# Kernel optimization log

Measured on AMD Instinct MI355X. Metric: run time of the kernel, lower is better.

The kernel has to match this reference:

```python
import jax, jax.numpy as jnp
import numpy as np

M_INST = 64   # num_instances (labels 1..64; 0 = background)
L_ANCH = 8    # anchors per instance
C_DIM = 256   # anchor_dim == embed dim (num_mapping_layers=0, num_heads=1)
B, H, W = 8, 64, 64


def setup_inputs() -> dict:
    key = jax.random.key(0)
    ks = jax.random.split(key, 7)
    s = 1.0 / np.sqrt(C_DIM)
    return {
        "anchors": jax.random.normal(ks[0], (M_INST, L_ANCH, C_DIM), jnp.float32),
        "features": jax.random.normal(ks[1], (B, H, W, C_DIM), jnp.float32),
        "instances_in_view": jax.random.randint(ks[2], (B, H, W), 0, M_INST + 1, jnp.int32),
        # nn.MultiheadAttention packed in-projection and out-projection params
        "in_proj_w": jax.random.normal(ks[3], (3 * C_DIM, C_DIM), jnp.float32) * s,
        "in_proj_b": jax.random.normal(ks[4], (3 * C_DIM,), jnp.float32) * s,
        "out_w": jax.random.normal(ks[5], (C_DIM, C_DIM), jnp.float32) * s,
        "out_b": jax.random.normal(ks[6], (C_DIM,), jnp.float32) * s,
    }


def reference(anchors, features, instances_in_view, in_proj_w, in_proj_b, out_w, out_b):
    # Cross-attention anchor_type, Identity maps (num_mapping_layers=0, num_heads=1).
    # Each pixel (query) attends to the L anchors of its instance; padding in the
    # original pad_sequence pipeline never affects non-pad queries, so the
    # gather/pack -> MHA -> unmap -> residual-add pipeline reduces to per-pixel math.
    C = anchors.shape[-1]
    Wq, Wk, Wv = in_proj_w[:C], in_proj_w[C:2 * C], in_proj_w[2 * C:]
    bq, bk, bv = in_proj_b[:C], in_proj_b[C:2 * C], in_proj_b[2 * C:]

    # Project keys/values once per instance: (M, L, C)
    K = jnp.einsum('mlc,dc->mld', anchors, Wk) + bk
    V = jnp.einsum('mlc,dc->mld', anchors, Wv) + bv

    Bsz, Hh, Ww, _ = features.shape
    f = features.reshape(-1, C)                       # (N, C)
    lab = instances_in_view.reshape(-1)               # (N,) labels 0..M
    idx = jnp.maximum(lab - 1, 0)                     # anchor row per pixel

    q = f @ Wq.T + bq                                 # (N, C)
    Kg = K[idx]                                       # (N, L, C) irregular gather
    Vg = V[idx]                                       # (N, L, C)

    scale = 1.0 / np.sqrt(C).astype(np.float32)
    scores = jnp.einsum('nc,nlc->nl', q, Kg) * scale  # (N, L)
    attn = jax.nn.softmax(scores, axis=-1)
    o = jnp.einsum('nl,nlc->nc', attn, Vg)            # (N, C)
    o = o @ out_w.T + out_b                           # MHA out_proj

    # background (label 0) pixels get zero anchor feature; residual add
    o = jnp.where((lab > 0)[:, None], o, jnp.zeros((), o.dtype))
    out = f + o
    return out.reshape(Bsz, Hh, Ww, C)
```

## Files before the change

### kernel.cpp

```cpp
#include <hip/hip_runtime.h>
#include <stdint.h>

#define C_DIM   256
#define L_ANCH  8
#define M_INST  64
#define NPIX    32768
#define LDSTR   264
#define WSTR    40
#define TSTR    80

typedef __attribute__((ext_vector_type(8))) short  short8;
typedef __attribute__((ext_vector_type(4))) float  float4v;

__device__ __forceinline__ float bf2f(unsigned short b) {
    union { unsigned u; float f; } x; x.u = ((unsigned)b) << 16; return x.f;
}
__device__ __forceinline__ unsigned short f2bf(float f) {
    union { unsigned u; float f; } x; x.f = f;
    unsigned u = x.u;
    return (unsigned short)((u + 0x7FFFu + ((u >> 16) & 1u)) >> 16);
}
__device__ __forceinline__ ushort4 f4bf(float4 f) {
    ushort4 v; v.x = f2bf(f.x); v.y = f2bf(f.y); v.z = f2bf(f.z); v.w = f2bf(f.w);
    return v;
}

__global__ __launch_bounds__(256) void prep1_kernel(
    const float* __restrict__ anchors, const float* __restrict__ in_proj_w,
    const float* __restrict__ in_proj_b, const float* __restrict__ out_w,
    unsigned short* __restrict__ Kb, unsigned short* __restrict__ Vb,
    unsigned short* __restrict__ WqT, unsigned short* __restrict__ Owb)
{
    __shared__ unsigned short Abuf[32 * LDSTR];
    __shared__ unsigned short Wtile[4][64 * WSTR];
    __shared__ unsigned short Ttile[64 * TSTR];
    const int b = blockIdx.x, t = threadIdx.x;

    if (b >= 96) {
        const int tidx = b - 96;
        const int r0 = (tidx >> 2) * 64, c0 = (tidx & 3) * 64;
#pragma unroll
        for (int i = 0; i < 4; ++i) {
            int id = t + i * 256;
            int row = id >> 4, c4 = id & 15;
            float4 f = *(const float4*)&in_proj_w[(size_t)(r0 + row) * C_DIM + c0 + c4 * 4];
            Ttile[(c4 * 4 + 0) * TSTR + row] = f2bf(f.x);
            Ttile[(c4 * 4 + 1) * TSTR + row] = f2bf(f.y);
            Ttile[(c4 * 4 + 2) * TSTR + row] = f2bf(f.z);
            Ttile[(c4 * 4 + 3) * TSTR + row] = f2bf(f.w);
        }
        __syncthreads();
#pragma unroll
        for (int i = 0; i < 2; ++i) {
            int id = t + i * 256;
            int cc = id >> 3, ch = id & 7;
            *(short8*)&WqT[(size_t)(c0 + cc) * C_DIM + r0 + ch * 8] =
                *(const short8*)&Ttile[cc * TSTR + ch * 8];
        }
        return;
    }

    if (b >= 32) {
        const int id = (b - 32) * 256 + t;
        float4 f = *((const float4*)out_w + id);
        *((ushort4*)Owb + id) = f4bf(f);
        return;
    }

    const int mat = b >> 4, tile = b & 15, m0 = tile * 32;
#pragma unroll
    for (int i = 0; i < 8; ++i) {
        int id = t + i * 256;
        int row = id >> 6, c4 = id & 63;
        float4 f = *((const float4*)(anchors + (size_t)(m0 + row) * C_DIM) + c4);
        *(ushort4*)&Abuf[row * LDSTR + c4 * 4] = f4bf(f);
    }
    __syncthreads();

    const int wave = t >> 6, lane = t & 63, r16 = lane & 15, quad = lane >> 4;
    const int wbase = C_DIM + mat * C_DIM + wave * 64;
    unsigned short* Wl = &Wtile[wave][0];

    float4v acc[2][4];
#pragma unroll
    for (int mt = 0; mt < 2; ++mt)
#pragma unroll
        for (int nt = 0; nt < 4; ++nt)
#pragma unroll
            for (int r = 0; r < 4; ++r) acc[mt][nt][r] = 0.f;

    for (int ks = 0; ks < 8; ++ks) {
        const int rr = lane >> 3, cc = lane & 7;
#pragma unroll
        for (int i = 0; i < 8; ++i) {
            int row = rr + i * 8;
            float4 f = *((const float4*)(in_proj_w + (size_t)(wbase + row) * C_DIM + ks * 32) + cc);
            *(ushort4*)&Wl[row * WSTR + cc * 4] = f4bf(f);
        }
        const int c0 = ks * 32 + quad * 8;
        short8 afr[2], bfr[4];
#pragma unroll
        for (int mt = 0; mt < 2; ++mt)
            afr[mt] = *(const short8*)&Abuf[(mt * 16 + r16) * LDSTR + c0];
#pragma unroll
        for (int nt = 0; nt < 4; ++nt)
            bfr[nt] = *(const short8*)&Wl[(nt * 16 + r16) * WSTR + quad * 8];
#pragma unroll
        for (int mt = 0; mt < 2; ++mt)
#pragma unroll
            for (int nt = 0; nt < 4; ++nt)
                acc[mt][nt] = __builtin_amdgcn_mfma_f32_16x16x32_bf16(
                    afr[mt], bfr[nt], acc[mt][nt], 0, 0, 0);
    }

    unsigned short* dst = mat ? Vb : Kb;
#pragma unroll
    for (int nt = 0; nt < 4; ++nt) {
        const int col = wave * 64 + nt * 16 + r16;
        const float bias = in_proj_b[C_DIM + mat * C_DIM + col];
#pragma unroll
        for (int mt = 0; mt < 2; ++mt)
#pragma unroll
            for (int r = 0; r < 4; ++r) {
                int row = m0 + mt * 16 + quad * 4 + r;
                dst[(size_t)row * C_DIM + col] = f2bf(acc[mt][nt][r] + bias);
            }
    }
}

__global__ __launch_bounds__(256) void prep2_kernel(
    const unsigned short* __restrict__ Kb, const unsigned short* __restrict__ Vb,
    const unsigned short* __restrict__ WqT, const unsigned short* __restrict__ Owb,
    const float* __restrict__ in_proj_b,
    unsigned short* __restrict__ G, unsigned short* __restrict__ U,
    float* __restrict__ g0)
{
    __shared__ unsigned short Abuf[32 * LDSTR];
    const int b = blockIdx.x, t = threadIdx.x;
    const int isG = (b < 16) ? 1 : 0;
    const int tile = b & 15, m0 = tile * 32;
    const unsigned short* src = isG ? Kb : Vb;
    const unsigned short* W   = isG ? WqT : Owb;
    unsigned short* dst       = isG ? G : U;

#pragma unroll
    for (int i = 0; i < 4; ++i) {
        int id = t + i * 256;
        int row = id >> 5, c8 = id & 31;
        *(short8*)&Abuf[row * LDSTR + c8 * 8] =
            *(const short8*)&src[(size_t)(m0 + row) * C_DIM + c8 * 8];
    }
    __syncthreads();

    const int wave = t >> 6, lane = t & 63, r16 = lane & 15, quad = lane >> 4;

    if (isG) {
        const int grow = t >> 3, gs = t & 7;
        float gp = 0.f;
#pragma unroll
        for (int c = 0; c < 32; ++c)
            gp += bf2f(Abuf[grow * LDSTR + gs * 32 + c]) * in_proj_b[gs * 32 + c];
        gp += __shfl_down(gp, 1);
        gp += __shfl_down(gp, 2);
        gp += __shfl_down(gp, 4);
        if (gs == 0) g0[m0 + grow] = gp;
    }

    float4v acc[2][4];
#pragma unroll
    for (int mt = 0; mt < 2; ++mt)
#pragma unroll
        for (int nt = 0; nt < 4; ++nt)
#pragma unroll
            for (int r = 0; r < 4; ++r) acc[mt][nt][r] = 0.f;

    for (int ks = 0; ks < 8; ++ks) {
        const int c0 = ks * 32 + quad * 8;
        short8 afr[2], bfr[4];
#pragma unroll
        for (int mt = 0; mt < 2; ++mt)
            afr[mt] = *(const short8*)&Abuf[(mt * 16 + r16) * LDSTR + c0];
#pragma unroll
        for (int nt = 0; nt < 4; ++nt)
            bfr[nt] = *(const short8*)&W[(size_t)(wave * 64 + nt * 16 + r16) * C_DIM + c0];
#pragma unroll
        for (int mt = 0; mt < 2; ++mt)
#pragma unroll
            for (int nt = 0; nt < 4; ++nt)
                acc[mt][nt] = __builtin_amdgcn_mfma_f32_16x16x32_bf16(
                    afr[mt], bfr[nt], acc[mt][nt], 0, 0, 0);
    }

#pragma unroll
    for (int nt = 0; nt < 4; ++nt) {
        const int col = wave * 64 + nt * 16 + r16;
#pragma unroll
        for (int mt = 0; mt < 2; ++mt)
#pragma unroll
            for (int r = 0; r < 4; ++r) {
                int row = m0 + mt * 16 + quad * 4 + r;
                dst[(size_t)row * C_DIM + col] = f2bf(acc[mt][nt][r]);
            }
    }
}

__global__ __launch_bounds__(256) void gather_kernel(
    const float* __restrict__ features, const int* __restrict__ inst,
    const float* __restrict__ out_b,
    const unsigned short* __restrict__ G, const unsigned short* __restrict__ U,
    const float* __restrict__ g0, float* __restrict__ out)
{
    const int t = threadIdx.x;
    const int p = t >> 3, s = t & 7;
    const int n = blockIdx.x * 32 + p;
    const int lab = inst[n];
    const int m = max(lab - 1, 0);
    const unsigned short* Gp = G + (size_t)m * (L_ANCH * C_DIM) + s * 32;
    const unsigned short* Up = U + (size_t)m * (L_ANCH * C_DIM) + s * 32;

    float fr[32];
    const float4* fp = (const float4*)(features + (size_t)n * C_DIM + s * 32);
#pragma unroll
    for (int i = 0; i < 8; ++i) *(float4*)&fr[i * 4] = fp[i];

    float sc[L_ANCH];
#pragma unroll
    for (int l = 0; l < L_ANCH; ++l) {
        short8 gv0 = *(const short8*)(Gp + l * C_DIM);
        short8 gv1 = *(const short8*)(Gp + l * C_DIM + 8);
        short8 gv2 = *(const short8*)(Gp + l * C_DIM + 16);
        short8 gv3 = *(const short8*)(Gp + l * C_DIM + 24);
        float a0 = 0.f, a1 = 0.f, a2 = 0.f, a3 = 0.f;
#pragma unroll
        for (int j = 0; j < 8; ++j) {
            a0 += bf2f(((const unsigned short*)&gv0)[j]) * fr[j];
            a1 += bf2f(((const unsigned short*)&gv1)[j]) * fr[8 + j];
            a2 += bf2f(((const unsigned short*)&gv2)[j]) * fr[16 + j];
            a3 += bf2f(((const unsigned short*)&gv3)[j]) * fr[24 + j];
        }
        float partial = (a0 + a1) + (a2 + a3);
        partial += __shfl_down(partial, 1);
        partial += __shfl_down(partial, 2);
        partial += __shfl_down(partial, 4);
        sc[l] = partial;
    }

    float attn[L_ANCH];
    if (s == 0) {
        const float scale = 0.0625f;
        float mx = -1e30f;
#pragma unroll
        for (int l = 0; l < L_ANCH; ++l) {
            sc[l] = (sc[l] + g0[m * L_ANCH + l]) * scale;
            mx = fmaxf(mx, sc[l]);
        }
        float sum = 0.f;
#pragma unroll
        for (int l = 0; l < L_ANCH; ++l) { attn[l] = __expf(sc[l] - mx); sum += attn[l]; }
        float inv = 1.f / sum;
#pragma unroll
        for (int l = 0; l < L_ANCH; ++l) attn[l] *= inv;
    }
    const int base_lane = (t & 63) & ~7;
    float a_bc[L_ANCH];
#pragma unroll
    for (int l = 0; l < L_ANCH; ++l) a_bc[l] = __shfl(attn[l], base_lane);

    float y[32];
#pragma unroll
    for (int c = 0; c < 32; ++c) y[c] = 0.f;
#pragma unroll
    for (int l = 0; l < L_ANCH; ++l) {
        const float av = a_bc[l];
        short8 uv0 = *(const short8*)(Up + l * C_DIM);
        short8 uv1 = *(const short8*)(Up + l * C_DIM + 8);
        short8 uv2 = *(const short8*)(Up + l * C_DIM + 16);
        short8 uv3 = *(const short8*)(Up + l * C_DIM + 24);
#pragma unroll
        for (int j = 0; j < 8; ++j) {
            y[j]      += av * bf2f(((const unsigned short*)&uv0)[j]);
            y[8 + j]  += av * bf2f(((const unsigned short*)&uv1)[j]);
            y[16 + j] += av * bf2f(((const unsigned short*)&uv2)[j]);
            y[24 + j] += av * bf2f(((const unsigned short*)&uv3)[j]);
        }
    }

    float4* op = (float4*)(out + (size_t)n * C_DIM + s * 32);
    const float4* obp = (const float4*)(out_b + s * 32);
#pragma unroll
    for (int i = 0; i < 8; ++i) {
        float4 ob = obp[i];
        float4 o;
        o.x = fr[i * 4 + 0] + ((lab > 0) ? (y[i * 4 + 0] + ob.x) : 0.f);
        o.y = fr[i * 4 + 1] + ((lab > 0) ? (y[i * 4 + 1] + ob.y) : 0.f);
        o.z = fr[i * 4 + 2] + ((lab > 0) ? (y[i * 4 + 2] + ob.z) : 0.f);
        o.w = fr[i * 4 + 3] + ((lab > 0) ? (y[i * 4 + 3] + ob.w) : 0.f);
        op[i] = o;
    }
}

extern "C" void kernel_launch(void* const* d_in, const int* in_sizes, int n_in,
                              void* d_out, int out_size, void* d_ws, size_t ws_size,
                              hipStream_t stream) {
    const float* anchors   = (const float*)d_in[0];
    const float* features  = (const float*)d_in[1];
    const int*   inst      = (const int*)d_in[2];
    const float* in_proj_w = (const float*)d_in[3];
    const float* in_proj_b = (const float*)d_in[4];
    const float* out_w     = (const float*)d_in[5];
    const float* out_b     = (const float*)d_in[6];
    float* out = (float*)d_out;

    unsigned short* Kb  = (unsigned short*)d_ws;
    unsigned short* Vb  = Kb  + M_INST * L_ANCH * C_DIM;
    unsigned short* WqT = Vb  + M_INST * L_ANCH * C_DIM;
    unsigned short* Owb = WqT + C_DIM * C_DIM;
    unsigned short* G   = Owb + C_DIM * C_DIM;
    unsigned short* U   = G   + M_INST * L_ANCH * C_DIM;
    float*          g0  = (float*)(U + M_INST * L_ANCH * C_DIM);

    prep1_kernel<<<112, 256, 0, stream>>>(anchors, in_proj_w, in_proj_b, out_w,
                                          Kb, Vb, WqT, Owb);
    prep2_kernel<<<32, 256, 0, stream>>>(Kb, Vb, WqT, Owb, in_proj_b, G, U, g0);
    gather_kernel<<<NPIX / 32, 256, 0, stream>>>(features, inst, out_b, G, U, g0, out);
}
```

Measured before the change: 136.2 us.

## Split prep GEMMs across column halves and halve per-thread gather work

The two small prep kernels now split each 32-row tile's output columns into two halves handled by separate blocks, doubling the block count so more CUs take part in the latency-bound weight-folding GEMMs. The gather kernel assigns 16 threads per pixel instead of 8, each handling 16 channels, which cuts per-thread registers and doubles the grid for more memory-level parallelism. The cost is an extra shuffle stage in the score reduction, and the anchor tile is loaded redundantly by both half-blocks.

```diff
diff --git a/kernel.cpp b/kernel.cpp
--- a/kernel.cpp
+++ b/kernel.cpp
@@ -32,12 +32,12 @@
     unsigned short* __restrict__ WqT, unsigned short* __restrict__ Owb)
 {
     __shared__ unsigned short Abuf[32 * LDSTR];
-    __shared__ unsigned short Wtile[4][64 * WSTR];
+    __shared__ unsigned short Wtile[4][32 * WSTR];
     __shared__ unsigned short Ttile[64 * TSTR];
     const int b = blockIdx.x, t = threadIdx.x;
 
-    if (b >= 96) {
-        const int tidx = b - 96;
+    if (b >= 128) {
+        const int tidx = b - 128;
         const int r0 = (tidx >> 2) * 64, c0 = (tidx & 3) * 64;
 #pragma unroll
         for (int i = 0; i < 4; ++i) {
@@ -60,14 +60,15 @@
         return;
     }
 
-    if (b >= 32) {
-        const int id = (b - 32) * 256 + t;
+    if (b >= 64) {
+        const int id = (b - 64) * 256 + t;
         float4 f = *((const float4*)out_w + id);
         *((ushort4*)Owb + id) = f4bf(f);
         return;
     }
 
-    const int mat = b >> 4, tile = b & 15, m0 = tile * 32;
+    const int mat = b >> 5, tile = (b >> 1) & 15, half = b & 1;
+    const int m0 = tile * 32;
 #pragma unroll
     for (int i = 0; i < 8; ++i) {
         int id = t + i * 256;
@@ -78,45 +79,46 @@
     __syncthreads();
 
     const int wave = t >> 6, lane = t & 63, r16 = lane & 15, quad = lane >> 4;
-    const int wbase = C_DIM + mat * C_DIM + wave * 64;
+    const int colbase = half * 128 + wave * 32;
+    const int wbase = C_DIM + mat * C_DIM + colbase;
     unsigned short* Wl = &Wtile[wave][0];
 
-    float4v acc[2][4];
+    float4v acc[2][2];
 #pragma unroll
     for (int mt = 0; mt < 2; ++mt)
 #pragma unroll
-        for (int nt = 0; nt < 4; ++nt)
+        for (int nt = 0; nt < 2; ++nt)
 #pragma unroll
             for (int r = 0; r < 4; ++r) acc[mt][nt][r] = 0.f;
 
     for (int ks = 0; ks < 8; ++ks) {
         const int rr = lane >> 3, cc = lane & 7;
 #pragma unroll
-        for (int i = 0; i < 8; ++i) {
+        for (int i = 0; i < 4; ++i) {
             int row = rr + i * 8;
             float4 f = *((const float4*)(in_proj_w + (size_t)(wbase + row) * C_DIM + ks * 32) + cc);
             *(ushort4*)&Wl[row * WSTR + cc * 4] = f4bf(f);
         }
         const int c0 = ks * 32 + quad * 8;
-        short8 afr[2], bfr[4];
+        short8 afr[2], bfr[2];
 #pragma unroll
         for (int mt = 0; mt < 2; ++mt)
             afr[mt] = *(const short8*)&Abuf[(mt * 16 + r16) * LDSTR + c0];
 #pragma unroll
-        for (int nt = 0; nt < 4; ++nt)
+        for (int nt = 0; nt < 2; ++nt)
             bfr[nt] = *(const short8*)&Wl[(nt * 16 + r16) * WSTR + quad * 8];
 #pragma unroll
         for (int mt = 0; mt < 2; ++mt)
 #pragma unroll
-            for (int nt = 0; nt < 4; ++nt)
+            for (int nt = 0; nt < 2; ++nt)
                 acc[mt][nt] = __builtin_amdgcn_mfma_f32_16x16x32_bf16(
                     afr[mt], bfr[nt], acc[mt][nt], 0, 0, 0);
     }
 
     unsigned short* dst = mat ? Vb : Kb;
 #pragma unroll
-    for (int nt = 0; nt < 4; ++nt) {
-        const int col = wave * 64 + nt * 16 + r16;
+    for (int nt = 0; nt < 2; ++nt) {
+        const int col = colbase + nt * 16 + r16;
         const float bias = in_proj_b[C_DIM + mat * C_DIM + col];
 #pragma unroll
         for (int mt = 0; mt < 2; ++mt)
@@ -137,8 +139,9 @@
 {
     __shared__ unsigned short Abuf[32 * LDSTR];
     const int b = blockIdx.x, t = threadIdx.x;
-    const int isG = (b < 16) ? 1 : 0;
-    const int tile = b & 15, m0 = tile * 32;
+    const int isG = (b < 32) ? 1 : 0;
+    const int tile = (b >> 1) & 15, half = b & 1;
+    const int m0 = tile * 32;
     const unsigned short* src = isG ? Kb : Vb;
     const unsigned short* W   = isG ? WqT : Owb;
     unsigned short* dst       = isG ? G : U;
@@ -154,7 +157,7 @@
 
     const int wave = t >> 6, lane = t & 63, r16 = lane & 15, quad = lane >> 4;
 
-    if (isG) {
+    if (isG && half == 0) {
         const int grow = t >> 3, gs = t & 7;
         float gp = 0.f;
 #pragma unroll
@@ -166,34 +169,36 @@
         if (gs == 0) g0[m0 + grow] = gp;
     }
 
-    float4v acc[2][4];
+    const int colbase = half * 128 + wave * 32;
+
+    float4v acc[2][2];
 #pragma unroll
     for (int mt = 0; mt < 2; ++mt)
 #pragma unroll
-        for (int nt = 0; nt < 4; ++nt)
+        for (int nt = 0; nt < 2; ++nt)
 #pragma unroll
             for (int r = 0; r < 4; ++r) acc[mt][nt][r] = 0.f;
 
     for (int ks = 0; ks < 8; ++ks) {
         const int c0 = ks * 32 + quad * 8;
-        short8 afr[2], bfr[4];
+        short8 afr[2], bfr[2];
 #pragma unroll
         for (int mt = 0; mt < 2; ++mt)
             afr[mt] = *(const short8*)&Abuf[(mt * 16 + r16) * LDSTR + c0];
 #pragma unroll
-        for (int nt = 0; nt < 4; ++nt)
-            bfr[nt] = *(const short8*)&W[(size_t)(wave * 64 + nt * 16 + r16) * C_DIM + c0];
-#pragma unroll
-        for (int mt = 0; mt < 2; ++mt)
-#pragma unroll
-            for (int nt = 0; nt < 4; ++nt)
+        for (int nt = 0; nt < 2; ++nt)
+            bfr[nt] = *(const short8*)&W[(size_t)(colbase + nt * 16 + r16) * C_DIM + c0];
+#pragma unroll
+        for (int mt = 0; mt < 2; ++mt)
+#pragma unroll
+            for (int nt = 0; nt < 2; ++nt)
                 acc[mt][nt] = __builtin_amdgcn_mfma_f32_16x16x32_bf16(
                     afr[mt], bfr[nt], acc[mt][nt], 0, 0, 0);
     }
 
 #pragma unroll
-    for (int nt = 0; nt < 4; ++nt) {
-        const int col = wave * 64 + nt * 16 + r16;
+    for (int nt = 0; nt < 2; ++nt) {
+        const int col = colbase + nt * 16 + r16;
 #pragma unroll
         for (int mt = 0; mt < 2; ++mt)
 #pragma unroll
@@ -211,37 +216,34 @@
     const float* __restrict__ g0, float* __restrict__ out)
 {
     const int t = threadIdx.x;
-    const int p = t >> 3, s = t & 7;
-    const int n = blockIdx.x * 32 + p;
+    const int p = t >> 4, s = t & 15;
+    const int n = blockIdx.x * 16 + p;
     const int lab = inst[n];
     const int m = max(lab - 1, 0);
-    const unsigned short* Gp = G + (size_t)m * (L_ANCH * C_DIM) + s * 32;
-    const unsigned short* Up = U + (size_t)m * (L_ANCH * C_DIM) + s * 32;
-
-    float fr[32];
-    const float4* fp = (const float4*)(features + (size_t)n * C_DIM + s * 32);
-#pragma unroll
-    for (int i = 0; i < 8; ++i) *(float4*)&fr[i * 4] = fp[i];
+    const unsigned short* Gp = G + (size_t)m * (L_ANCH * C_DIM) + s * 16;
+    const unsigned short* Up = U + (size_t)m * (L_ANCH * C_DIM) + s * 16;
+
+    float fr[16];
+    const float4* fp = (const float4*)(features + (size_t)n * C_DIM + s * 16);
+#pragma unroll
+    for (int i = 0; i < 4; ++i) *(float4*)&fr[i * 4] = fp[i];
 
     float sc[L_ANCH];
 #pragma unroll
     for (int l = 0; l < L_ANCH; ++l) {
         short8 gv0 = *(const short8*)(Gp + l * C_DIM);
         short8 gv1 = *(const short8*)(Gp + l * C_DIM + 8);
-        short8 gv2 = *(const short8*)(Gp + l * C_DIM + 16);
-        short8 gv3 = *(const short8*)(Gp + l * C_DIM + 24);
-        float a0 = 0.f, a1 = 0.f, a2 = 0.f, a3 = 0.f;
+        float a0 = 0.f, a1 = 0.f;
 #pragma unroll
         for (int j = 0; j < 8; ++j) {
             a0 += bf2f(((const unsigned short*)&gv0)[j]) * fr[j];
             a1 += bf2f(((const unsigned short*)&gv1)[j]) * fr[8 + j];
-            a2 += bf2f(((const unsigned short*)&gv2)[j]) * fr[16 + j];
-            a3 += bf2f(((const unsigned short*)&gv3)[j]) * fr[24 + j];
-        }
-        float partial = (a0 + a1) + (a2 + a3);
+        }
+        float partial = a0 + a1;
         partial += __shfl_down(partial, 1);
         partial += __shfl_down(partial, 2);
         partial += __shfl_down(partial, 4);
+        partial += __shfl_down(partial, 8);
         sc[l] = partial;
     }
 
@@ -261,40 +263,37 @@
 #pragma unroll
         for (int l = 0; l < L_ANCH; ++l) attn[l] *= inv;
     }
-    const int base_lane = (t & 63) & ~7;
+    const int base_lane = (t & 63) & ~15;
     float a_bc[L_ANCH];
 #pragma unroll
     for (int l = 0; l < L_ANCH; ++l) a_bc[l] = __shfl(attn[l], base_lane);
 
-    float y[32];
-#pragma unroll
-    for (int c = 0; c < 32; ++c) y[c] = 0.f;
+    float y[16];
+#pragma unroll
+    for (int c = 0; c < 16; ++c) y[c] = 0.f;
 #pragma unroll
     for (int l = 0; l < L_ANCH; ++l) {
         const float av = a_bc[l];
         short8 uv0 = *(const short8*)(Up + l * C_DIM);
         short8 uv1 = *(const short8*)(Up + l * C_DIM + 8);
-        short8 uv2 = *(const short8*)(Up + l * C_DIM + 16);
-        short8 uv3 = *(const short8*)(Up + l * C_DIM + 24);
 #pragma unroll
         for (int j = 0; j < 8; ++j) {
-            y[j]      += av * bf2f(((const unsigned short*)&uv0)[j]);
-            y[8 + j]  += av * bf2f(((const unsigned short*)&uv1)[j]);
-            y[16 + j] += av * bf2f(((const unsigned short*)&uv2)[j]);
-            y[24 + j] += av * bf2f(((const unsigned short*)&uv3)[j]);
-        }
-    }
-
-    float4* op = (float4*)(out + (size_t)n * C_DIM + s * 32);
-    const float4* obp = (const float4*)(out_b + s * 32);
-#pragma unroll
-    for (int i = 0; i < 8; ++i) {
+            y[j]     += av * bf2f(((const unsigned short*)&uv0)[j]);
+            y[8 + j] += av * bf2f(((const unsigned short*)&uv1)[j]);
+        }
+    }
+
+    const float fm = (lab > 0) ? 1.f : 0.f;
+    float4* op = (float4*)(out + (size_t)n * C_DIM + s * 16);
+    const float4* obp = (const float4*)(out_b + s * 16);
+#pragma unroll
+    for (int i = 0; i < 4; ++i) {
         float4 ob = obp[i];
         float4 o;
-        o.x = fr[i * 4 + 0] + ((lab > 0) ? (y[i * 4 + 0] + ob.x) : 0.f);
-        o.y = fr[i * 4 + 1] + ((lab > 0) ? (y[i * 4 + 1] + ob.y) : 0.f);
-        o.z = fr[i * 4 + 2] + ((lab > 0) ? (y[i * 4 + 2] + ob.z) : 0.f);
-        o.w = fr[i * 4 + 3] + ((lab > 0) ? (y[i * 4 + 3] + ob.w) : 0.f);
+        o.x = fr[i * 4 + 0] + fm * (y[i * 4 + 0] + ob.x);
+        o.y = fr[i * 4 + 1] + fm * (y[i * 4 + 1] + ob.y);
+        o.z = fr[i * 4 + 2] + fm * (y[i * 4 + 2] + ob.z);
+        o.w = fr[i * 4 + 3] + fm * (y[i * 4 + 3] + ob.w);
         op[i] = o;
     }
 }
@@ -319,8 +318,8 @@
     unsigned short* U   = G   + M_INST * L_ANCH * C_DIM;
     float*          g0  = (float*)(U + M_INST * L_ANCH * C_DIM);
 
-    prep1_kernel<<<112, 256, 0, stream>>>(anchors, in_proj_w, in_proj_b, out_w,
+    prep1_kernel<<<144, 256, 0, stream>>>(anchors, in_proj_w, in_proj_b, out_w,
                                           Kb, Vb, WqT, Owb);
-    prep2_kernel<<<32, 256, 0, stream>>>(Kb, Vb, WqT, Owb, in_proj_b, G, U, g0);
-    gather_kernel<<<NPIX / 32, 256, 0, stream>>>(features, inst, out_b, G, U, g0, out);
-}
+    prep2_kernel<<<64, 256, 0, stream>>>(Kb, Vb, WqT, Owb, in_proj_b, G, U, g0);
+    gather_kernel<<<NPIX / 16, 256, 0, stream>>>(features, inst, out_b, G, U, g0, out);
+}
```

New measurement: 122.4 us. -10.1%, faster.
